# Performance work log

Measured on AMD Instinct MI355X. Metric: run time of the kernel, lower is better.

Reference implementation:

```python
import jax, jax.numpy as jnp
import numpy as np

B, D, rL, rD, d = 512, 960, 16, 32, 512
LP, LH = 16, 384
R_PH = 0.7
dP = int(round(R_PH * d))  # 358
dH = d - dP                # 154
BN_EPS = 1e-5


def _xavier(key, shape):
    limit = float(np.sqrt(6.0 / (shape[0] + shape[1])))
    return jax.random.uniform(key, shape, jnp.float32, -limit, limit)


def _prefix_mask(key, batch, L_pad):
    # contiguous prefix masks: Lb uniform in [1, L_pad]
    lens = jax.random.randint(key, (batch,), 1, L_pad + 1)
    return (jnp.arange(L_pad)[None, :] < lens[:, None]).astype(jnp.int32)


def setup_inputs() -> dict:
    key = jax.random.key(0)
    ks = jax.random.split(key, 24)
    inp = {
        "emb_P": jax.random.normal(ks[0], (B, LP, D), jnp.float32),
        "emb_H": jax.random.normal(ks[1], (B, LH, D), jnp.float32),
        "mask_P": _prefix_mask(ks[2], B, LP),
        "mask_H": _prefix_mask(ks[3], B, LH),
        # peptide encoder params
        "B_cP": _xavier(ks[4], (D, rD)),
        "A_cP": _xavier(ks[5], (LP, rL)),
        "H_cP": _xavier(ks[6], (rL * rD, dP)),
        "W1P": _xavier(ks[7], (dP, dP)), "b1P": jnp.zeros((dP,), jnp.float32),
        "gP": jnp.ones((dP,), jnp.float32), "betaP": jnp.zeros((dP,), jnp.float32),
        "W2P": _xavier(ks[8], (dP, dP)), "b2P": jnp.zeros((dP,), jnp.float32),
        # HLA encoder params
        "B_cH": _xavier(ks[9], (D, rD)),
        "A_cH": _xavier(ks[10], (LH, rL)),
        "H_cH": _xavier(ks[11], (rL * rD, dH)),
        "W1H": _xavier(ks[12], (dH, dH)), "b1H": jnp.zeros((dH,), jnp.float32),
        "gH": jnp.ones((dH,), jnp.float32), "betaH": jnp.zeros((dH,), jnp.float32),
        "W2H": _xavier(ks[13], (dH, dH)), "b2H": jnp.zeros((dH,), jnp.float32),
    }
    return inp


def _encode(emb, mask, B_c, A_c, H_c, W1, b1, g, beta, W2, b2):
    # masked low-rank projection; equivalent to the per-sample ragged loop
    # for contiguous prefix masks (A_c rows align with padded positions).
    Xm = emb * mask[..., None].astype(emb.dtype)            # (B, L, D)
    Y = jnp.einsum("bld,dr->blr", Xm, B_c)                  # (B, L, rD)
    U = jnp.einsum("lp,blr->bpr", A_c, Y)                   # (B, rL, rD)
    z = U.reshape(U.shape[0], -1) @ H_c                     # (B, d_mod)
    # expander (eval mode: BN uses running stats mean=0/var=1; dropout off)
    h = z @ W1 + b1
    h = h * (g / jnp.sqrt(1.0 + BN_EPS)) + beta
    h = jax.nn.relu(h)
    return h @ W2 + b2


def reference(emb_P, emb_H, B_cP, A_cP, H_cP, W1P, b1P, gP, betaP, W2P, b2P,
              B_cH, A_cH, H_cH, W1H, b1H, gH, betaH, W2H, b2H,
              mask_P, mask_H):
    zP = _encode(emb_P, mask_P, B_cP, A_cP, H_cP, W1P, b1P, gP, betaP, W2P, b2P)
    zH = _encode(emb_H, mask_H, B_cH, A_cH, H_cH, W1H, b1H, gH, betaH, W2H, b2H)
    return jnp.concatenate([zP, zH], axis=-1)  # (B, d)
```

## Files before the change

### kernel.cpp

```cpp
#include <hip/hip_runtime.h>
#include <cstddef>

constexpr int Bn  = 512;
constexpr int Dd  = 960;
constexpr int RL  = 16;
constexpr int RD  = 32;
constexpr int LPp = 16;
constexpr int LHh = 384;
constexpr int DP  = 358;
constexpr int DH  = 154;
constexpr int CH  = 128;

typedef float f32x4 __attribute__((ext_vector_type(4)));

struct EncParams {
    const float* X;
    const int*   mask;
    const float* A;
    const float* Bc;
    const float* Hc;
    const float* W1; const float* b1; const float* g; const float* beta;
    const float* W2; const float* b2;
    int L, dmod, ooff;
};

__global__ void zero_kernel(int* __restrict__ q)
{
    if (threadIdx.x == 0) *q = 0;
}

__global__ __launch_bounds__(512)
void persist_kernel(EncParams H, EncParams P, int* __restrict__ qcnt,
                    float* __restrict__ out)
{
    const int t = threadIdx.x;
    __shared__ float Vs[RL][Dd];
    __shared__ float As[CH * RL];
    __shared__ float Ush[RL * RD];
    __shared__ int   s_item, s_len;

    const int  g   = t >> 8;
    const int  w   = t & 255;
    const bool act = (w < 240);
    const int  col = 4 * w;

    for (;;) {
        __syncthreads();
        if (t == 0) { s_item = atomicAdd(qcnt, 1); s_len = 0; }
        __syncthreads();
        const int item = s_item;
        if (item >= 2 * Bn) return;
        const bool isH = (item < Bn);
        const EncParams E = isH ? H : P;
        const int b = isH ? item : item - Bn;

        int loc = 0;
        for (int i = t; i < E.L; i += 512) loc += E.mask[(size_t)b * E.L + i];
        if (loc) atomicAdd(&s_len, loc);
        __syncthreads();
        const int len = s_len;

        float v[RL][4];
        #pragma unroll
        for (int p = 0; p < RL; ++p)
            { v[p][0] = 0.f; v[p][1] = 0.f; v[p][2] = 0.f; v[p][3] = 0.f; }

        const float* Xb = E.X + (size_t)b * E.L * Dd;

        for (int c0 = 0; c0 < len; c0 += CH) {
            __syncthreads();
            {
                const int row = c0 + (t >> 2);
                f32x4 av = {0.f, 0.f, 0.f, 0.f};
                if (row < len)
                    av = *(const f32x4*)(E.A + (size_t)row * RL + (t & 3) * 4);
                *(f32x4*)&As[(t >> 2) * RL + (t & 3) * 4] = av;
            }
            __syncthreads();

            if (act) {
                const int lim = min(len, c0 + CH);
                int l = c0 + g;
                if (l < lim) {
                    const float* rp = Xb + (size_t)l * Dd + col;
                    f32x4 x = __builtin_nontemporal_load((const f32x4*)rp);
                    for (; l < lim; l += 2) {
                        f32x4 xn = x;
                        if (l + 2 < lim) {
                            rp += 2 * (size_t)Dd;
                            xn = __builtin_nontemporal_load((const f32x4*)rp);
                        }
                        float a[RL];
                        const int lr = l - c0;
                        *(f32x4*)&a[0]  = *(const f32x4*)&As[lr * RL + 0];
                        *(f32x4*)&a[4]  = *(const f32x4*)&As[lr * RL + 4];
                        *(f32x4*)&a[8]  = *(const f32x4*)&As[lr * RL + 8];
                        *(f32x4*)&a[12] = *(const f32x4*)&As[lr * RL + 12];
                        #pragma unroll
                        for (int p = 0; p < RL; ++p) {
                            v[p][0] = fmaf(a[p], x[0], v[p][0]);
                            v[p][1] = fmaf(a[p], x[1], v[p][1]);
                            v[p][2] = fmaf(a[p], x[2], v[p][2]);
                            v[p][3] = fmaf(a[p], x[3], v[p][3]);
                        }
                        x = xn;
                    }
                }
            }
        }

        __syncthreads();
        if (g == 0 && act) {
            #pragma unroll
            for (int p = 0; p < RL; ++p)
                *(f32x4*)&Vs[p][col] = *(f32x4*)&v[p][0];
        }
        __syncthreads();
        if (g == 1 && act) {
            #pragma unroll
            for (int p = 0; p < RL; ++p) {
                f32x4 cur = *(const f32x4*)&Vs[p][col];
                cur += *(f32x4*)&v[p][0];
                *(f32x4*)&Vs[p][col] = cur;
            }
        }
        __syncthreads();

        {
            const int p = t >> 5, r = t & 31;
            float u0 = 0.f, u1 = 0.f;
            for (int dd = 0; dd < Dd; dd += 8) {
                f32x4 va = *(const f32x4*)&Vs[p][dd];
                f32x4 vb = *(const f32x4*)&Vs[p][dd + 4];
                #pragma unroll
                for (int q = 0; q < 4; ++q) {
                    u0 = fmaf(va[q], E.Bc[(size_t)(dd + q) * RD + r],     u0);
                    u1 = fmaf(vb[q], E.Bc[(size_t)(dd + 4 + q) * RD + r], u1);
                }
            }
            Ush[t] = u0 + u1;
        }
        __syncthreads();

        float* zs = &Vs[0][0];
        float* hs = zs + 512;
        for (int j = t; j < E.dmod; j += 512) {
            float a0 = 0.f, a1 = 0.f, a2 = 0.f, a3 = 0.f;
            #pragma unroll 4
            for (int i = 0; i < RL * RD; i += 4) {
                a0 = fmaf(Ush[i],     E.Hc[(size_t)i * E.dmod + j],       a0);
                a1 = fmaf(Ush[i + 1], E.Hc[(size_t)(i + 1) * E.dmod + j], a1);
                a2 = fmaf(Ush[i + 2], E.Hc[(size_t)(i + 2) * E.dmod + j], a2);
                a3 = fmaf(Ush[i + 3], E.Hc[(size_t)(i + 3) * E.dmod + j], a3);
            }
            zs[j] = (a0 + a1) + (a2 + a3);
        }
        __syncthreads();

        const float bscale = rsqrtf(1.f + 1e-5f);
        const int K = E.dmod;
        for (int c = t; c < K; c += 512) {
            float a0 = E.b1[c], a1 = 0.f;
            #pragma unroll 4
            for (int k = 0; k < K; k += 2) {
                a0 = fmaf(zs[k],     E.W1[(size_t)k * K + c],       a0);
                a1 = fmaf(zs[k + 1], E.W1[(size_t)(k + 1) * K + c], a1);
            }
            float acc = a0 + a1;
            acc = fmaf(acc, E.g[c] * bscale, E.beta[c]);
            hs[c] = fmaxf(acc, 0.f);
        }
        __syncthreads();

        for (int c = t; c < K; c += 512) {
            float a0 = E.b2[c], a1 = 0.f;
            #pragma unroll 4
            for (int k = 0; k < K; k += 2) {
                a0 = fmaf(hs[k],     E.W2[(size_t)k * K + c],       a0);
                a1 = fmaf(hs[k + 1], E.W2[(size_t)(k + 1) * K + c], a1);
            }
            out[(size_t)b * (DP + DH) + E.ooff + c] = a0 + a1;
        }
    }
}

extern "C" void kernel_launch(void* const* d_in, const int* in_sizes, int n_in,
                              void* d_out, int out_size, void* d_ws, size_t ws_size,
                              hipStream_t stream)
{
    EncParams P, H;
    P.X    = (const float*)d_in[0];
    H.X    = (const float*)d_in[1];
    P.mask = (const int*)  d_in[2];
    H.mask = (const int*)  d_in[3];
    P.Bc   = (const float*)d_in[4];
    P.A    = (const float*)d_in[5];
    P.Hc   = (const float*)d_in[6];
    P.W1   = (const float*)d_in[7];
    P.b1   = (const float*)d_in[8];
    P.g    = (const float*)d_in[9];
    P.beta = (const float*)d_in[10];
    P.W2   = (const float*)d_in[11];
    P.b2   = (const float*)d_in[12];
    H.Bc   = (const float*)d_in[13];
    H.A    = (const float*)d_in[14];
    H.Hc   = (const float*)d_in[15];
    H.W1   = (const float*)d_in[16];
    H.b1   = (const float*)d_in[17];
    H.g    = (const float*)d_in[18];
    H.beta = (const float*)d_in[19];
    H.W2   = (const float*)d_in[20];
    H.b2   = (const float*)d_in[21];
    P.L = LPp;  P.dmod = DP;  P.ooff = 0;
    H.L = LHh;  H.dmod = DH;  H.ooff = DP;

    float* outp = (float*)d_out;
    int*   qcnt = (int*)d_ws;

    zero_kernel<<<dim3(1), dim3(64), 0, stream>>>(qcnt);
    persist_kernel<<<dim3(512), dim3(512), 0, stream>>>(H, P, qcnt, outp);
}
```

Before: 215.2 us.

## Double-buffer X rows into LDS via async global_load_lds pipeline

Replaces the per-thread register-prefetched global loads of embedding rows with a double-buffered pipeline that stages 8-row chunks of X straight into shared memory using global_load_lds, overlapping the next chunk's fetch with the current chunk's FMAs. The A matrix is loaded once per item instead of per chunk, and the grid shrinks from 512 to 256 persistent blocks. The aim is to hide memory latency on the bandwidth-bound masked projection. In exchange the kernel relies on hand-written waitcnt and barrier ordering, uses more LDS per block, and clamps loads near the buffer end, so occupancy and latency hiding may change.

```diff
diff --git a/kernel.cpp b/kernel.cpp
--- a/kernel.cpp
+++ b/kernel.cpp
@@ -9,7 +9,8 @@
 constexpr int LHh = 384;
 constexpr int DP  = 358;
 constexpr int DH  = 154;
-constexpr int CH  = 128;
+constexpr int CR  = 8;
+constexpr int SLOTS = (CR * Dd) / 256;
 
 typedef float f32x4 __attribute__((ext_vector_type(4)));
 
@@ -19,8 +20,9 @@
     const float* A;
     const float* Bc;
     const float* Hc;
-    const float* W1; const float* b1; const float* g; const float* beta;
+    const float* W1; const float* b1; const float* gam; const float* beta;
     const float* W2; const float* b2;
+    const float* Xclamp;
     int L, dmod, ooff;
 };
 
@@ -34,15 +36,16 @@
                     float* __restrict__ out)
 {
     const int t = threadIdx.x;
-    __shared__ float Vs[RL][Dd];
-    __shared__ float As[CH * RL];
+    __shared__ float UXs[2 * CR * Dd];
+    __shared__ float As[(LHh + CR) * RL];
     __shared__ float Ush[RL * RD];
     __shared__ int   s_item, s_len;
 
-    const int  g   = t >> 8;
-    const int  w   = t & 255;
-    const bool act = (w < 240);
-    const int  col = 4 * w;
+    const int  grp  = t >> 8;
+    const int  w    = t & 255;
+    const bool act  = (w < 240);
+    const int  col  = 4 * w;
+    const int  wave = t >> 6;
 
     for (;;) {
         __syncthreads();
@@ -58,70 +61,89 @@
         for (int i = t; i < E.L; i += 512) loc += E.mask[(size_t)b * E.L + i];
         if (loc) atomicAdd(&s_len, loc);
         __syncthreads();
-        const int len = s_len;
+        const int len = __builtin_amdgcn_readfirstlane(s_len);
+
+        for (int i = t; i < (E.L + CR) * 4; i += 512) {
+            const int row = i >> 2, q4 = (i & 3) * 4;
+            f32x4 av = {0.f, 0.f, 0.f, 0.f};
+            if (row < len) av = *(const f32x4*)(E.A + (size_t)row * RL + q4);
+            *(f32x4*)&As[row * RL + q4] = av;
+        }
+        __syncthreads();
 
         float v[RL][4];
         #pragma unroll
         for (int p = 0; p < RL; ++p)
             { v[p][0] = 0.f; v[p][1] = 0.f; v[p][2] = 0.f; v[p][3] = 0.f; }
 
-        const float* Xb = E.X + (size_t)b * E.L * Dd;
-
-        for (int c0 = 0; c0 < len; c0 += CH) {
-            __syncthreads();
-            {
-                const int row = c0 + (t >> 2);
-                f32x4 av = {0.f, 0.f, 0.f, 0.f};
-                if (row < len)
-                    av = *(const f32x4*)(E.A + (size_t)row * RL + (t & 3) * 4);
-                *(f32x4*)&As[(t >> 2) * RL + (t & 3) * 4] = av;
-            }
-            __syncthreads();
-
+        const float* Xb  = E.X + (size_t)b * E.L * Dd;
+        const int    nch = (len + CR - 1) / CR;
+
+        auto stage = [&](int chunk, int buf) {
+            const float* cbase = Xb + (size_t)chunk * CR * Dd;
+            #pragma unroll
+            for (int i = 0; i < 4; ++i) {
+                int slot = wave * 4 + i;
+                if (slot >= SLOTS) slot -= 2;
+                const float* src = cbase + slot * 256 + (t & 63) * 4;
+                if (src > E.Xclamp) src = E.Xclamp;
+                __builtin_amdgcn_global_load_lds(
+                    (const __attribute__((address_space(1))) void*)src,
+                    (__attribute__((address_space(3))) void*)
+                        &UXs[buf * CR * Dd + slot * 256],
+                    16, 0, 0);
+            }
+        };
+
+        stage(0, 0);
+        for (int k = 0; k < nch; ++k) {
+            const int cb = k & 1;
+            if (k + 1 < nch) {
+                stage(k + 1, cb ^ 1);
+                asm volatile("s_waitcnt vmcnt(4)" ::: "memory");
+            } else {
+                asm volatile("s_waitcnt vmcnt(0)" ::: "memory");
+            }
+            __builtin_amdgcn_s_barrier();
+            __builtin_amdgcn_sched_barrier(0);
             if (act) {
-                const int lim = min(len, c0 + CH);
-                int l = c0 + g;
-                if (l < lim) {
-                    const float* rp = Xb + (size_t)l * Dd + col;
-                    f32x4 x = __builtin_nontemporal_load((const f32x4*)rp);
-                    for (; l < lim; l += 2) {
-                        f32x4 xn = x;
-                        if (l + 2 < lim) {
-                            rp += 2 * (size_t)Dd;
-                            xn = __builtin_nontemporal_load((const f32x4*)rp);
-                        }
-                        float a[RL];
-                        const int lr = l - c0;
-                        *(f32x4*)&a[0]  = *(const f32x4*)&As[lr * RL + 0];
-                        *(f32x4*)&a[4]  = *(const f32x4*)&As[lr * RL + 4];
-                        *(f32x4*)&a[8]  = *(const f32x4*)&As[lr * RL + 8];
-                        *(f32x4*)&a[12] = *(const f32x4*)&As[lr * RL + 12];
-                        #pragma unroll
-                        for (int p = 0; p < RL; ++p) {
-                            v[p][0] = fmaf(a[p], x[0], v[p][0]);
-                            v[p][1] = fmaf(a[p], x[1], v[p][1]);
-                            v[p][2] = fmaf(a[p], x[2], v[p][2]);
-                            v[p][3] = fmaf(a[p], x[3], v[p][3]);
-                        }
-                        x = xn;
+                const float* Xc = &UXs[cb * CR * Dd];
+                const int c0 = k * CR;
+                #pragma unroll
+                for (int rr = grp; rr < CR; rr += 2) {
+                    f32x4 x = *(const f32x4*)&Xc[rr * Dd + col];
+                    const float* ar = &As[(c0 + rr) * RL];
+                    float a[RL];
+                    *(f32x4*)&a[0]  = *(const f32x4*)(ar + 0);
+                    *(f32x4*)&a[4]  = *(const f32x4*)(ar + 4);
+                    *(f32x4*)&a[8]  = *(const f32x4*)(ar + 8);
+                    *(f32x4*)&a[12] = *(const f32x4*)(ar + 12);
+                    #pragma unroll
+                    for (int p = 0; p < RL; ++p) {
+                        v[p][0] = fmaf(a[p], x[0], v[p][0]);
+                        v[p][1] = fmaf(a[p], x[1], v[p][1]);
+                        v[p][2] = fmaf(a[p], x[2], v[p][2]);
+                        v[p][3] = fmaf(a[p], x[3], v[p][3]);
                     }
                 }
             }
-        }
-
-        __syncthreads();
-        if (g == 0 && act) {
+            __builtin_amdgcn_sched_barrier(0);
+            __builtin_amdgcn_s_barrier();
+        }
+
+        float* Vs = &UXs[0];
+        if (grp == 0 && act) {
             #pragma unroll
             for (int p = 0; p < RL; ++p)
-                *(f32x4*)&Vs[p][col] = *(f32x4*)&v[p][0];
-        }
-        __syncthreads();
-        if (g == 1 && act) {
+                *(f32x4*)&Vs[p * Dd + col] = *(f32x4*)&v[p][0];
+        }
+        __syncthreads();
+        if (grp == 1 && act) {
             #pragma unroll
             for (int p = 0; p < RL; ++p) {
-                f32x4 cur = *(const f32x4*)&Vs[p][col];
-                cur += *(f32x4*)&v[p][0];
-                *(f32x4*)&Vs[p][col] = cur;
+                f32x4 c = *(const f32x4*)&Vs[p * Dd + col];
+                c += *(f32x4*)&v[p][0];
+                *(f32x4*)&Vs[p * Dd + col] = c;
             }
         }
         __syncthreads();
@@ -130,8 +152,8 @@
             const int p = t >> 5, r = t & 31;
             float u0 = 0.f, u1 = 0.f;
             for (int dd = 0; dd < Dd; dd += 8) {
-                f32x4 va = *(const f32x4*)&Vs[p][dd];
-                f32x4 vb = *(const f32x4*)&Vs[p][dd + 4];
+                f32x4 va = *(const f32x4*)&Vs[p * Dd + dd];
+                f32x4 vb = *(const f32x4*)&Vs[p * Dd + dd + 4];
                 #pragma unroll
                 for (int q = 0; q < 4; ++q) {
                     u0 = fmaf(va[q], E.Bc[(size_t)(dd + q) * RD + r],     u0);
@@ -142,7 +164,7 @@
         }
         __syncthreads();
 
-        float* zs = &Vs[0][0];
+        float* zs = &UXs[0];
         float* hs = zs + 512;
         for (int j = t; j < E.dmod; j += 512) {
             float a0 = 0.f, a1 = 0.f, a2 = 0.f, a3 = 0.f;
@@ -167,7 +189,7 @@
                 a1 = fmaf(zs[k + 1], E.W1[(size_t)(k + 1) * K + c], a1);
             }
             float acc = a0 + a1;
-            acc = fmaf(acc, E.g[c] * bscale, E.beta[c]);
+            acc = fmaf(acc, E.gam[c] * bscale, E.beta[c]);
             hs[c] = fmaxf(acc, 0.f);
         }
         __syncthreads();
@@ -198,7 +220,7 @@
     P.Hc   = (const float*)d_in[6];
     P.W1   = (const float*)d_in[7];
     P.b1   = (const float*)d_in[8];
-    P.g    = (const float*)d_in[9];
+    P.gam  = (const float*)d_in[9];
     P.beta = (const float*)d_in[10];
     P.W2   = (const float*)d_in[11];
     P.b2   = (const float*)d_in[12];
@@ -207,16 +229,18 @@
     H.Hc   = (const float*)d_in[15];
     H.W1   = (const float*)d_in[16];
     H.b1   = (const float*)d_in[17];
-    H.g    = (const float*)d_in[18];
+    H.gam  = (const float*)d_in[18];
     H.beta = (const float*)d_in[19];
     H.W2   = (const float*)d_in[20];
     H.b2   = (const float*)d_in[21];
     P.L = LPp;  P.dmod = DP;  P.ooff = 0;
     H.L = LHh;  H.dmod = DH;  H.ooff = DP;
+    P.Xclamp = P.X + (size_t)in_sizes[0] - 4;
+    H.Xclamp = H.X + (size_t)in_sizes[1] - 4;
 
     float* outp = (float*)d_out;
     int*   qcnt = (int*)d_ws;
 
     zero_kernel<<<dim3(1), dim3(64), 0, stream>>>(qcnt);
-    persist_kernel<<<dim3(512), dim3(512), 0, stream>>>(H, P, qcnt, outp);
+    persist_kernel<<<dim3(256), dim3(512), 0, stream>>>(H, P, qcnt, outp);
 }
```

New measurement: 274.1 us, median of 6. 27.4% more time.

## Split per-sample dense tail into batched tiled GEMM kernels

Applied to the files above, without the earlier changes.

The persistent kernel now stops after the rank-reduction step and writes U to workspace. The H_c projection and both expander layers then run as three batched 64x64 tiled GEMM kernels across all samples. Previously every work item re-read the full H_c, W1 and W2 matrices per sample with scalar loops. The change also replaces the conditional prefetch in the streaming loop with a clamped unconditional load. In exchange it adds three kernel launches and workspace round-trips for the intermediates.

```diff
diff --git a/kernel.cpp b/kernel.cpp
--- a/kernel.cpp
+++ b/kernel.cpp
@@ -13,15 +13,12 @@
 
 typedef float f32x4 __attribute__((ext_vector_type(4)));
 
-struct EncParams {
+struct EncIn {
     const float* X;
     const int*   mask;
     const float* A;
     const float* Bc;
-    const float* Hc;
-    const float* W1; const float* b1; const float* g; const float* beta;
-    const float* W2; const float* b2;
-    int L, dmod, ooff;
+    int L;
 };
 
 __global__ void zero_kernel(int* __restrict__ q)
@@ -30,16 +27,15 @@
 }
 
 __global__ __launch_bounds__(512)
-void persist_kernel(EncParams H, EncParams P, int* __restrict__ qcnt,
-                    float* __restrict__ out)
+void stream_kernel(EncIn H, EncIn P, int* __restrict__ qcnt,
+                   float* __restrict__ Uws)
 {
     const int t = threadIdx.x;
     __shared__ float Vs[RL][Dd];
     __shared__ float As[CH * RL];
-    __shared__ float Ush[RL * RD];
     __shared__ int   s_item, s_len;
 
-    const int  g   = t >> 8;
+    const int  grp = t >> 8;
     const int  w   = t & 255;
     const bool act = (w < 240);
     const int  col = 4 * w;
@@ -51,7 +47,7 @@
         const int item = s_item;
         if (item >= 2 * Bn) return;
         const bool isH = (item < Bn);
-        const EncParams E = isH ? H : P;
+        const EncIn E = isH ? H : P;
         const int b = isH ? item : item - Bn;
 
         int loc = 0;
@@ -80,16 +76,16 @@
 
             if (act) {
                 const int lim = min(len, c0 + CH);
-                int l = c0 + g;
+                int l = c0 + grp;
                 if (l < lim) {
-                    const float* rp = Xb + (size_t)l * Dd + col;
+                    const float* rp    = Xb + (size_t)l * Dd + col;
+                    const float* rpmax = Xb + (size_t)(E.L - 1) * Dd + col;
                     f32x4 x = __builtin_nontemporal_load((const f32x4*)rp);
                     for (; l < lim; l += 2) {
-                        f32x4 xn = x;
-                        if (l + 2 < lim) {
-                            rp += 2 * (size_t)Dd;
-                            xn = __builtin_nontemporal_load((const f32x4*)rp);
-                        }
+                        const float* rp2 = rp + 2 * (size_t)Dd;
+                        rp2 = (rp2 > rpmax) ? rpmax : rp2;
+                        f32x4 xn = __builtin_nontemporal_load((const f32x4*)rp2);
+                        rp = rp2;
                         float a[RL];
                         const int lr = l - c0;
                         *(f32x4*)&a[0]  = *(const f32x4*)&As[lr * RL + 0];
@@ -110,13 +106,13 @@
         }
 
         __syncthreads();
-        if (g == 0 && act) {
+        if (grp == 0 && act) {
             #pragma unroll
             for (int p = 0; p < RL; ++p)
                 *(f32x4*)&Vs[p][col] = *(f32x4*)&v[p][0];
         }
         __syncthreads();
-        if (g == 1 && act) {
+        if (grp == 1 && act) {
             #pragma unroll
             for (int p = 0; p < RL; ++p) {
                 f32x4 cur = *(const f32x4*)&Vs[p][col];
@@ -129,6 +125,7 @@
         {
             const int p = t >> 5, r = t & 31;
             float u0 = 0.f, u1 = 0.f;
+            #pragma unroll 2
             for (int dd = 0; dd < Dd; dd += 8) {
                 f32x4 va = *(const f32x4*)&Vs[p][dd];
                 f32x4 vb = *(const f32x4*)&Vs[p][dd + 4];
@@ -138,48 +135,89 @@
                     u1 = fmaf(vb[q], E.Bc[(size_t)(dd + 4 + q) * RD + r], u1);
                 }
             }
-            Ush[t] = u0 + u1;
-        }
-        __syncthreads();
-
-        float* zs = &Vs[0][0];
-        float* hs = zs + 512;
-        for (int j = t; j < E.dmod; j += 512) {
-            float a0 = 0.f, a1 = 0.f, a2 = 0.f, a3 = 0.f;
-            #pragma unroll 4
-            for (int i = 0; i < RL * RD; i += 4) {
-                a0 = fmaf(Ush[i],     E.Hc[(size_t)i * E.dmod + j],       a0);
-                a1 = fmaf(Ush[i + 1], E.Hc[(size_t)(i + 1) * E.dmod + j], a1);
-                a2 = fmaf(Ush[i + 2], E.Hc[(size_t)(i + 2) * E.dmod + j], a2);
-                a3 = fmaf(Ush[i + 3], E.Hc[(size_t)(i + 3) * E.dmod + j], a3);
-            }
-            zs[j] = (a0 + a1) + (a2 + a3);
-        }
-        __syncthreads();
-
-        const float bscale = rsqrtf(1.f + 1e-5f);
-        const int K = E.dmod;
-        for (int c = t; c < K; c += 512) {
-            float a0 = E.b1[c], a1 = 0.f;
-            #pragma unroll 4
-            for (int k = 0; k < K; k += 2) {
-                a0 = fmaf(zs[k],     E.W1[(size_t)k * K + c],       a0);
-                a1 = fmaf(zs[k + 1], E.W1[(size_t)(k + 1) * K + c], a1);
-            }
-            float acc = a0 + a1;
-            acc = fmaf(acc, E.g[c] * bscale, E.beta[c]);
-            hs[c] = fmaxf(acc, 0.f);
-        }
-        __syncthreads();
-
-        for (int c = t; c < K; c += 512) {
-            float a0 = E.b2[c], a1 = 0.f;
-            #pragma unroll 4
-            for (int k = 0; k < K; k += 2) {
-                a0 = fmaf(hs[k],     E.W2[(size_t)k * K + c],       a0);
-                a1 = fmaf(hs[k + 1], E.W2[(size_t)(k + 1) * K + c], a1);
-            }
-            out[(size_t)b * (DP + DH) + E.ooff + c] = a0 + a1;
+            Uws[(size_t)item * 512 + t] = u0 + u1;
+        }
+    }
+}
+
+template <int MODE>
+__global__ __launch_bounds__(256)
+void gemm_kernel(const float* __restrict__ AaP, const float* __restrict__ WP,
+                 const float* __restrict__ biasP, const float* __restrict__ gPv,
+                 const float* __restrict__ betaPv, float* __restrict__ outP,
+                 const float* __restrict__ AaH, const float* __restrict__ WH,
+                 const float* __restrict__ biasH, const float* __restrict__ gHv,
+                 const float* __restrict__ betaHv, float* __restrict__ outH,
+                 int nbP, int KP, int NP, int KH, int NH)
+{
+    const float *Aa, *W, *bias, *g, *beta; float* out;
+    int K, N, n0, ooff;
+    if ((int)blockIdx.y < nbP) {
+        Aa = AaP; W = WP; bias = biasP; g = gPv; beta = betaPv; out = outP;
+        K = KP; N = NP; n0 = blockIdx.y * 64; ooff = 0;
+    } else {
+        Aa = AaH; W = WH; bias = biasH; g = gHv; beta = betaHv; out = outH;
+        K = KH; N = NH; n0 = (blockIdx.y - nbP) * 64; ooff = DP;
+    }
+
+    constexpr int TM = 64, TN = 64, KC = 32;
+    __shared__ float AsT[KC][TM + 4];
+    __shared__ float Ws[KC][TN];
+    const int t  = threadIdx.x;
+    const int m0 = blockIdx.x * TM;
+    const int r0 = (t >> 4) << 2;
+    const int c0 = (t & 15) << 2;
+    float acc[4][4] = {};
+
+    for (int k0 = 0; k0 < K; k0 += KC) {
+        for (int i = t; i < TM * KC; i += 256) {
+            int row = i >> 5, kk = i & 31;
+            int kg = k0 + kk;
+            AsT[kk][row] = (kg < K) ? Aa[(size_t)(m0 + row) * K + kg] : 0.f;
+        }
+        for (int i = t; i < KC * TN; i += 256) {
+            int kk = i >> 6, c = i & 63;
+            int kg = k0 + kk, cg = n0 + c;
+            Ws[kk][c] = (kg < K && cg < N) ? W[(size_t)kg * N + cg] : 0.f;
+        }
+        __syncthreads();
+        #pragma unroll
+        for (int kk = 0; kk < KC; ++kk) {
+            float4 av = *(const float4*)&AsT[kk][r0];
+            float4 wv = *(const float4*)&Ws[kk][c0];
+            const float a[4] = {av.x, av.y, av.z, av.w};
+            const float wv4[4] = {wv.x, wv.y, wv.z, wv.w};
+            #pragma unroll
+            for (int i = 0; i < 4; ++i)
+                #pragma unroll
+                for (int j = 0; j < 4; ++j)
+                    acc[i][j] = fmaf(a[i], wv4[j], acc[i][j]);
+        }
+        __syncthreads();
+    }
+
+    const float bscale = rsqrtf(1.f + 1e-5f);
+    #pragma unroll
+    for (int j = 0; j < 4; ++j) {
+        int c = n0 + c0 + j;
+        if (c < N) {
+            float bb = 0.f, gg = 0.f, be = 0.f;
+            if constexpr (MODE != 2) bb = bias[c];
+            if constexpr (MODE == 0) { gg = g[c] * bscale; be = beta[c]; }
+            #pragma unroll
+            for (int i = 0; i < 4; ++i) {
+                int m = m0 + r0 + i;
+                float vv = acc[i][j] + bb;
+                if constexpr (MODE == 0) {
+                    vv = fmaf(vv, gg, be);
+                    vv = fmaxf(vv, 0.f);
+                    out[(size_t)m * N + c] = vv;
+                } else if constexpr (MODE == 1) {
+                    out[(size_t)m * (DP + DH) + ooff + c] = vv;
+                } else {
+                    out[(size_t)m * N + c] = vv;
+                }
+            }
         }
     }
 }
@@ -188,35 +226,60 @@
                               void* d_out, int out_size, void* d_ws, size_t ws_size,
                               hipStream_t stream)
 {
-    EncParams P, H;
-    P.X    = (const float*)d_in[0];
-    H.X    = (const float*)d_in[1];
-    P.mask = (const int*)  d_in[2];
-    H.mask = (const int*)  d_in[3];
-    P.Bc   = (const float*)d_in[4];
-    P.A    = (const float*)d_in[5];
-    P.Hc   = (const float*)d_in[6];
-    P.W1   = (const float*)d_in[7];
-    P.b1   = (const float*)d_in[8];
-    P.g    = (const float*)d_in[9];
-    P.beta = (const float*)d_in[10];
-    P.W2   = (const float*)d_in[11];
-    P.b2   = (const float*)d_in[12];
-    H.Bc   = (const float*)d_in[13];
-    H.A    = (const float*)d_in[14];
-    H.Hc   = (const float*)d_in[15];
-    H.W1   = (const float*)d_in[16];
-    H.b1   = (const float*)d_in[17];
-    H.g    = (const float*)d_in[18];
-    H.beta = (const float*)d_in[19];
-    H.W2   = (const float*)d_in[20];
-    H.b2   = (const float*)d_in[21];
-    P.L = LPp;  P.dmod = DP;  P.ooff = 0;
-    H.L = LHh;  H.dmod = DH;  H.ooff = DP;
-
+    const float* emb_P  = (const float*)d_in[0];
+    const float* emb_H  = (const float*)d_in[1];
+    const int*   mask_P = (const int*)  d_in[2];
+    const int*   mask_H = (const int*)  d_in[3];
+    const float* B_cP   = (const float*)d_in[4];
+    const float* A_cP   = (const float*)d_in[5];
+    const float* H_cP   = (const float*)d_in[6];
+    const float* W1P    = (const float*)d_in[7];
+    const float* b1P    = (const float*)d_in[8];
+    const float* gP     = (const float*)d_in[9];
+    const float* betaP  = (const float*)d_in[10];
+    const float* W2P    = (const float*)d_in[11];
+    const float* b2P    = (const float*)d_in[12];
+    const float* B_cH   = (const float*)d_in[13];
+    const float* A_cH   = (const float*)d_in[14];
+    const float* H_cH   = (const float*)d_in[15];
+    const float* W1H    = (const float*)d_in[16];
+    const float* b1H    = (const float*)d_in[17];
+    const float* gH     = (const float*)d_in[18];
+    const float* betaH  = (const float*)d_in[19];
+    const float* W2H    = (const float*)d_in[20];
+    const float* b2H    = (const float*)d_in[21];
     float* outp = (float*)d_out;
+
     int*   qcnt = (int*)d_ws;
+    float* U_ws = (float*)d_ws + 256;
+    float* z_P  = U_ws + (size_t)2 * Bn * 512;
+    float* z_H  = z_P + (size_t)Bn * DP;
+    float* h_P  = z_H + (size_t)Bn * DH;
+    float* h_H  = h_P + (size_t)Bn * DP;
+
+    EncIn Hin, Pin;
+    Hin.X = emb_H; Hin.mask = mask_H; Hin.A = A_cH; Hin.Bc = B_cH; Hin.L = LHh;
+    Pin.X = emb_P; Pin.mask = mask_P; Pin.A = A_cP; Pin.Bc = B_cP; Pin.L = LPp;
 
     zero_kernel<<<dim3(1), dim3(64), 0, stream>>>(qcnt);
-    persist_kernel<<<dim3(512), dim3(512), 0, stream>>>(H, P, qcnt, outp);
-}
+
+    stream_kernel<<<dim3(512), dim3(512), 0, stream>>>(Hin, Pin, qcnt, U_ws);
+
+    const float* U_H = U_ws;
+    const float* U_P = U_ws + (size_t)Bn * 512;
+
+    gemm_kernel<2><<<dim3(8, 9), dim3(256), 0, stream>>>(
+        U_P, H_cP, nullptr, nullptr, nullptr, z_P,
+        U_H, H_cH, nullptr, nullptr, nullptr, z_H,
+        6, 512, DP, 512, DH);
+
+    gemm_kernel<0><<<dim3(8, 9), dim3(256), 0, stream>>>(
+        z_P, W1P, b1P, gP, betaP, h_P,
+        z_H, W1H, b1H, gH, betaH, h_H,
+        6, DP, DP, DH, DH);
+
+    gemm_kernel<1><<<dim3(8, 9), dim3(256), 0, stream>>>(
+        h_P, W2P, b2P, nullptr, nullptr, outp,
+        h_H, W2H, b2H, nullptr, nullptr, outp,
+        6, DP, DP, DH, DH);
+}
```

Result: slower. 327.8 us (+52.4%).
